# Kernel optimization log

Measured on AMD Instinct MI355X. Metric: run time of the kernel, lower is better.

## Reference

```python
import jax, jax.numpy as jnp
import numpy as np

RANK = 32
NC = 32                      # n_components = out_features / rank = 1024/32
TRI = RANK * (RANK + 1) // 2  # 528
EPS = 1e-5


def setup_inputs() -> dict:
    key = jax.random.key(0)
    k1, k2, k3, k4, k5 = jax.random.split(key, 5)
    B, T, D = 2, 2048, 1024
    param_arg = jax.random.normal(k1, (B, T, D), dtype=jnp.float32)
    input_arg = jax.random.normal(k2, (B, T, D), dtype=jnp.float32)
    # learned params (weight_norm linears collapse to plain weight matrices)
    W_uv = jax.random.normal(k3, (NC * TRI, D), dtype=jnp.float32) * 0.02
    W_alpha = jax.random.normal(k4, (NC, D), dtype=jnp.float32) * 0.02
    b_alpha = jax.random.normal(k5, (NC,), dtype=jnp.float32) * 0.02
    return {"param_arg": param_arg, "input_arg": input_arg,
            "W_uv": W_uv, "W_alpha": W_alpha, "b_alpha": b_alpha}


def reference(param_arg, input_arg, W_uv, W_alpha, b_alpha):
    B, T, D = input_arg.shape
    N = B * T * NC
    # projections (mixer_ac = identity)
    params = jnp.einsum('btd,pd->btp', param_arg, W_uv)            # [B,T,NC*TRI]
    alpha = jax.nn.sigmoid(jnp.einsum('btd,cd->btc', param_arg, W_alpha) + b_alpha)  # [B,T,NC]
    p = params.reshape(N, TRI)
    iu, ju = jnp.triu_indices(RANK)
    uv = jnp.zeros((N, RANK, RANK), dtype=p.dtype).at[:, iu, ju].set(p)
    uv = jnp.einsum('nij,nkj->nik', uv, uv)                        # U U^T, symmetric PSD
    # per-column L2 norm (dim=-2), then max over columns
    col = jnp.sqrt(jnp.sum(uv * uv, axis=-2, keepdims=True))       # [N,1,RANK]
    uv = uv / (jnp.max(col, axis=-1, keepdims=True) + EPS)
    x = input_arg.reshape(N, RANK)                                 # (-1, rank, 1)
    y = alpha.reshape(N, 1) * jnp.einsum('nij,nj->ni', uv, x)      # [N,RANK]
    return input_arg - y.reshape(B, T, D)
```

## Files before the change

kernel.cpp:

```cpp
#include <hip/hip_runtime.h>
#include <hip/hip_bf16.h>
#include <stdint.h>

typedef float f32x4 __attribute__((ext_vector_type(4)));
typedef float f32x16 __attribute__((ext_vector_type(16)));
typedef __bf16 bf16x8 __attribute__((ext_vector_type(8)));

#define EPS 1e-5f

static __device__ __forceinline__ unsigned short f2bf(float f) {
  unsigned int u = __float_as_uint(f);
  unsigned int r = (u + 0x7fffu + ((u >> 16) & 1u)) >> 16;
  return (unsigned short)r;
}

static __device__ __forceinline__ void gload_lds16(const unsigned short* g, unsigned short* s) {
  __builtin_amdgcn_global_load_lds((const __attribute__((address_space(1))) unsigned int*)g,
                                   (__attribute__((address_space(3))) unsigned int*)s,
                                   16, 0, 0);
}

__global__ void k_convert(const float* __restrict__ src, unsigned short* __restrict__ dst, int n4) {
  int idx = blockIdx.x * blockDim.x + threadIdx.x;
  int stride = gridDim.x * blockDim.x;
  for (int i = idx; i < n4; i += stride) {
    f32x4 v = ((const f32x4*)src)[i];
    ushort4 o;
    o.x = f2bf(v.x); o.y = f2bf(v.y); o.z = f2bf(v.z); o.w = f2bf(v.w);
    ((ushort4*)dst)[i] = o;
  }
}

__global__ __launch_bounds__(256) void k_alpha(const float* __restrict__ A,
                                               const float* __restrict__ Wa,
                                               const float* __restrict__ ba,
                                               float* __restrict__ alpha,
                                               unsigned short* __restrict__ Ab) {
  __shared__ __align__(16) float arow[1024];
  const int bt = blockIdx.x, tid = threadIdx.x;
  f32x4 v = ((const f32x4*)(A + (size_t)bt * 1024))[tid];
  ((f32x4*)arow)[tid] = v;
  ushort4 o;
  o.x = f2bf(v.x); o.y = f2bf(v.y); o.z = f2bf(v.z); o.w = f2bf(v.w);
  ((ushort4*)(Ab + (size_t)bt * 1024))[tid] = o;
  __syncthreads();
  const int c = tid >> 3, h = tid & 7;
  const float* wr = Wa + (size_t)c * 1024 + h * 128;
  const float* ar = arow + h * 128;
  float s = 0.f;
#pragma unroll 8
  for (int j = 0; j < 128; j += 4) {
    f32x4 wv = *(const f32x4*)(wr + j);
    s += wv.x * ar[j] + wv.y * ar[j + 1] + wv.z * ar[j + 2] + wv.w * ar[j + 3];
  }
  s += __shfl_down(s, 4);
  s += __shfl_down(s, 2);
  s += __shfl_down(s, 1);
  if (h == 0) {
    float z = s + ba[c];
    alpha[(size_t)bt * 32 + c] = 1.f / (1.f + __expf(-z));
  }
}

__global__ __launch_bounds__(256) void k_gemm(const unsigned short* __restrict__ A,
                                              const unsigned short* __restrict__ W,
                                              unsigned short* __restrict__ C) {
  __shared__ __align__(16) unsigned short As[4096];
  __shared__ __align__(16) unsigned short Bs[4096];
  const int bid = blockIdx.x;
  const int tm = bid / 132, tn = bid - tm * 132;
  const int m0 = tm << 7, n0 = tn << 7;
  const int tid = threadIdx.x;
  const int lane = tid & 63;
  const int w = tid >> 6;
  const int wm = w >> 1, wn = w & 1;
  const int fr = lane & 15, fq = lane >> 4;

  f32x4 acc[4][4];
#pragma unroll
  for (int i = 0; i < 4; ++i)
#pragma unroll
    for (int j = 0; j < 4; ++j) acc[i][j] = (f32x4){0.f, 0.f, 0.f, 0.f};

  const int srow = (w << 5) + (lane >> 2);
  const int scol = (lane & 3) << 3;
  const unsigned short* gA = A + (size_t)(m0 + srow) * 1024 + scol;
  const unsigned short* gB = W + (size_t)(n0 + srow) * 1024 + scol;

  for (int k0 = 0; k0 < 1024; k0 += 32) {
#pragma unroll
    for (int i = 0; i < 2; ++i) {
      gload_lds16(gA + (size_t)(i * 16) * 1024 + k0, &As[(w << 10) + (i << 9)]);
      gload_lds16(gB + (size_t)(i * 16) * 1024 + k0, &Bs[(w << 10) + (i << 9)]);
    }
    __syncthreads();
    bf16x8 af[4], bfr[4];
#pragma unroll
    for (int mi = 0; mi < 4; ++mi)
      af[mi] = *(const bf16x8*)&As[((wm << 6) + (mi << 4) + fr) * 32 + (fq << 3)];
#pragma unroll
    for (int ni = 0; ni < 4; ++ni)
      bfr[ni] = *(const bf16x8*)&Bs[((wn << 6) + (ni << 4) + fr) * 32 + (fq << 3)];
#pragma unroll
    for (int mi = 0; mi < 4; ++mi)
#pragma unroll
      for (int ni = 0; ni < 4; ++ni)
        acc[mi][ni] = __builtin_amdgcn_mfma_f32_16x16x32_bf16(af[mi], bfr[ni], acc[mi][ni], 0, 0, 0);
    __syncthreads();
  }

#pragma unroll
  for (int mi = 0; mi < 4; ++mi)
#pragma unroll
    for (int ni = 0; ni < 4; ++ni)
#pragma unroll
      for (int r = 0; r < 4; ++r) {
        int row = m0 + (wm << 6) + (mi << 4) + (fq << 2) + r;
        int col = n0 + (wn << 6) + (ni << 4) + fr;
        C[(size_t)row * 16896 + col] = f2bf(acc[mi][ni][r]);
      }
}

__global__ __launch_bounds__(256) void k_epi(const unsigned short* __restrict__ P,
                                             const float* __restrict__ X,
                                             const float* __restrict__ alpha,
                                             float* __restrict__ out) {
  __shared__ __align__(16) unsigned short U[4][1280];
  __shared__ __align__(16) float Xl[4][32];
  __shared__ unsigned short tab[528];
  const int tid = threadIdx.x;
  for (int e = tid; e < 528; e += 256) {
    float fi = (65.0f - sqrtf((float)(4225 - 8 * e))) * 0.5f;
    int i = (int)fi;
    int oi = (i * (65 - i)) >> 1;
    if (e < oi) { --i; oi = (i * (65 - i)) >> 1; }
    else { int oi1 = ((i + 1) * (64 - i)) >> 1; if (e >= oi1) { oi = oi1; ++i; } }
    tab[e] = (unsigned short)(i * 40 + i + (e - oi));
  }
  const int w = tid >> 6, lane = tid & 63;
  const int n = (blockIdx.x << 2) + w;
  const int bt = n >> 5, c = n & 31;
  unsigned short* Uw = U[w];
#pragma unroll
  for (int t = 0; t < 5; ++t) ((ushort4*)Uw)[lane + (t << 6)] = make_ushort4(0, 0, 0, 0);
  if (lane < 32) Xl[w][lane] = X[(size_t)bt * 1024 + (c << 5) + lane];
  __syncthreads();

  const unsigned short* p = P + (size_t)bt * 16896 + c * 528;
#pragma unroll
  for (int e = 0; e < 9; ++e) {
    int idx = lane + (e << 6);
    if (idx < 528) Uw[tab[idx]] = p[idx];
  }

  const int col = lane & 31, hi = lane >> 5;
  bf16x8 fa0 = *(const bf16x8*)&Uw[col * 40 + (hi << 3)];
  bf16x8 fa1 = *(const bf16x8*)&Uw[col * 40 + 16 + (hi << 3)];
  f32x16 S = {0.f, 0.f, 0.f, 0.f, 0.f, 0.f, 0.f, 0.f, 0.f, 0.f, 0.f, 0.f, 0.f, 0.f, 0.f, 0.f};
  S = __builtin_amdgcn_mfma_f32_32x32x16_bf16(fa0, fa0, S, 0, 0, 0);
  S = __builtin_amdgcn_mfma_f32_32x32x16_bf16(fa1, fa1, S, 0, 0, 0);

  float css = 0.f;
#pragma unroll
  for (int r = 0; r < 16; ++r) css += S[r] * S[r];
  css += __shfl_xor(css, 32);
  float m = css;
#pragma unroll
  for (int off = 1; off < 32; off <<= 1) m = fmaxf(m, __shfl_xor(m, off));
  m = sqrtf(m);
  const float scale = alpha[n] / (m + EPS);

  const float* xw = Xl[w];
  f32x4 x0 = *(const f32x4*)&xw[(hi << 2)];
  f32x4 x1 = *(const f32x4*)&xw[8 + (hi << 2)];
  f32x4 x2 = *(const f32x4*)&xw[16 + (hi << 2)];
  f32x4 x3 = *(const f32x4*)&xw[24 + (hi << 2)];
  float y = 0.f;
#pragma unroll
  for (int r = 0; r < 4; ++r) y += x0[r] * S[r];
#pragma unroll
  for (int r = 0; r < 4; ++r) y += x1[r] * S[4 + r];
#pragma unroll
  for (int r = 0; r < 4; ++r) y += x2[r] * S[8 + r];
#pragma unroll
  for (int r = 0; r < 4; ++r) y += x3[r] * S[12 + r];
  y += __shfl_xor(y, 32);

  if (hi == 0) {
    out[(size_t)bt * 1024 + (c << 5) + col] = xw[col] - scale * y;
  }
}

extern "C" void kernel_launch(void* const* d_in, const int* in_sizes, int n_in,
                              void* d_out, int out_size, void* d_ws, size_t ws_size,
                              hipStream_t stream) {
  const float* param = (const float*)d_in[0];
  const float* input = (const float*)d_in[1];
  const float* W_uv  = (const float*)d_in[2];
  const float* W_al  = (const float*)d_in[3];
  const float* b_al  = (const float*)d_in[4];
  float* out = (float*)d_out;

  char* ws = (char*)d_ws;
  unsigned short* Ab    = (unsigned short*)(ws);
  unsigned short* Wb    = (unsigned short*)(ws + 8388608);
  float*          alpha = (float*)(ws + 42991616);
  unsigned short* Pp    = (unsigned short*)(ws + 43515904);

  k_convert<<<4096, 256, 0, stream>>>(W_uv, Wb, (16896 * 1024) / 4);
  k_alpha<<<4096, 256, 0, stream>>>(param, W_al, b_al, alpha, Ab);
  k_gemm<<<32 * 132, 256, 0, stream>>>(Ab, Wb, Pp);
  k_epi<<<131072 / 4, 256, 0, stream>>>(Pp, input, alpha, out);
}
```

Measured before the change: 310.6 us.

## Replace bf16 GEMM with 256x256-tile double-buffered, swizzled, phase-pipelined kernel

```diff
diff --git a/kernel.cpp b/kernel.cpp
--- a/kernel.cpp
+++ b/kernel.cpp
@@ -62,62 +62,128 @@
   }
 }
 
-__global__ __launch_bounds__(256) void k_gemm(const unsigned short* __restrict__ A,
-                                              const unsigned short* __restrict__ W,
-                                              unsigned short* __restrict__ C) {
-  __shared__ __align__(16) unsigned short As[4096];
-  __shared__ __align__(16) unsigned short Bs[4096];
+
+#define SWZ(b) ((b) ^ ((((b) >> 9) & 3) << 5))
+
+#define STAGE(S, h) do {                                                        \
+  const int _buf = (S) & 1;                                                     \
+  const int _reg = _buf * 65536 + (((h) >= 2) ? ((h) - 2) * 16384               \
+                                              : 32768 + (h) * 16384);           \
+  const unsigned short* _mat = ((h) >= 2) ? A : W;                              \
+  const int _r0 = (((h) >= 2) ? m0 : n0) + ((h) & 1) * 128;                     \
+  const int _kb = (S) * 128;                                                    \
+  _Pragma("unroll")                                                             \
+  for (int _l = 0; _l < 2; ++_l) {                                              \
+    int _db = _l * 8192 + tid * 16;                                             \
+    int _sb = SWZ(_db);                                                         \
+    gload_lds16((const unsigned short*)((const char*)_mat +                     \
+                    (size_t)(_r0 + (_sb >> 7)) * 2048 + _kb + (_sb & 127)),     \
+                (unsigned short*)(smem + _reg + _l * 8192 + wid * 1024));       \
+  } } while (0)
+
+#define READ_A(buf, qm) do {                                                    \
+  _Pragma("unroll") for (int _mi = 0; _mi < 4; ++_mi)                           \
+  _Pragma("unroll") for (int _ks = 0; _ks < 2; ++_ks) {                         \
+    int _b = ((qm) * 64 + _mi * 16 + fr) * 128 + _ks * 64 + fq * 16;            \
+    _b = SWZ(_b);                                                               \
+    af[_mi][_ks] = *(const bf16x8*)(smem + (buf) * 65536 + wm * 16384 + _b);    \
+  } } while (0)
+
+#define READ_B(buf, qn) do {                                                    \
+  _Pragma("unroll") for (int _ni = 0; _ni < 2; ++_ni)                           \
+  _Pragma("unroll") for (int _ks = 0; _ks < 2; ++_ks) {                         \
+    int _b = ((wn & 1) * 64 + (qn) * 32 + _ni * 16 + fr) * 128 + _ks * 64 + fq * 16; \
+    _b = SWZ(_b);                                                               \
+    bfr[qn][_ni][_ks] = *(const bf16x8*)(smem + (buf) * 65536 + 32768 +         \
+                                         (wn >> 1) * 16384 + _b);               \
+  } } while (0)
+
+#define MMA(qm, qn) do {                                                        \
+  __builtin_amdgcn_s_setprio(1);                                                \
+  _Pragma("unroll") for (int _mi = 0; _mi < 4; ++_mi)                           \
+  _Pragma("unroll") for (int _ni = 0; _ni < 2; ++_ni)                           \
+  _Pragma("unroll") for (int _ks = 0; _ks < 2; ++_ks)                           \
+    acc[(qm) * 4 + _mi][(qn) * 2 + _ni] = __builtin_amdgcn_mfma_f32_16x16x32_bf16( \
+        af[_mi][_ks], bfr[qn][_ni][_ks], acc[(qm) * 4 + _mi][(qn) * 2 + _ni], 0, 0, 0); \
+  __builtin_amdgcn_s_setprio(0);                                                \
+  } while (0)
+
+#define PH_SYNC do {                                                            \
+  __builtin_amdgcn_s_barrier();                                                 \
+  asm volatile("s_waitcnt lgkmcnt(0)" ::: "memory");                            \
+  __builtin_amdgcn_sched_barrier(0);                                            \
+  } while (0)
+
+#define ENDBAR __builtin_amdgcn_s_barrier()
+#define VMW4 asm volatile("s_waitcnt vmcnt(4)" ::: "memory")
+#define LGKM8 asm volatile("s_waitcnt lgkmcnt(8)" ::: "memory")
+
+__global__ __launch_bounds__(512, 2) void k_gemm8(const unsigned short* __restrict__ A,
+                                                  const unsigned short* __restrict__ W,
+                                                  unsigned short* __restrict__ C) {
+  extern __shared__ char smem[];
   const int bid = blockIdx.x;
-  const int tm = bid / 132, tn = bid - tm * 132;
-  const int m0 = tm << 7, n0 = tn << 7;
+  const int tm = bid / 66, tn = bid - tm * 66;
+  const int m0 = tm << 8, n0 = tn << 8;
   const int tid = threadIdx.x;
   const int lane = tid & 63;
-  const int w = tid >> 6;
-  const int wm = w >> 1, wn = w & 1;
+  const int wid = tid >> 6;
+  const int wm = wid >> 2, wn = wid & 3;
   const int fr = lane & 15, fq = lane >> 4;
 
-  f32x4 acc[4][4];
-#pragma unroll
-  for (int i = 0; i < 4; ++i)
+  f32x4 acc[8][4];
+#pragma unroll
+  for (int i = 0; i < 8; ++i)
 #pragma unroll
     for (int j = 0; j < 4; ++j) acc[i][j] = (f32x4){0.f, 0.f, 0.f, 0.f};
 
-  const int srow = (w << 5) + (lane >> 2);
-  const int scol = (lane & 3) << 3;
-  const unsigned short* gA = A + (size_t)(m0 + srow) * 1024 + scol;
-  const unsigned short* gB = W + (size_t)(n0 + srow) * 1024 + scol;
-
-  for (int k0 = 0; k0 < 1024; k0 += 32) {
-#pragma unroll
-    for (int i = 0; i < 2; ++i) {
-      gload_lds16(gA + (size_t)(i * 16) * 1024 + k0, &As[(w << 10) + (i << 9)]);
-      gload_lds16(gB + (size_t)(i * 16) * 1024 + k0, &Bs[(w << 10) + (i << 9)]);
-    }
-    __syncthreads();
-    bf16x8 af[4], bfr[4];
-#pragma unroll
-    for (int mi = 0; mi < 4; ++mi)
-      af[mi] = *(const bf16x8*)&As[((wm << 6) + (mi << 4) + fr) * 32 + (fq << 3)];
-#pragma unroll
-    for (int ni = 0; ni < 4; ++ni)
-      bfr[ni] = *(const bf16x8*)&Bs[((wn << 6) + (ni << 4) + fr) * 32 + (fq << 3)];
-#pragma unroll
-    for (int mi = 0; mi < 4; ++mi)
-#pragma unroll
-      for (int ni = 0; ni < 4; ++ni)
-        acc[mi][ni] = __builtin_amdgcn_mfma_f32_16x16x32_bf16(af[mi], bfr[ni], acc[mi][ni], 0, 0, 0);
-    __syncthreads();
-  }
-
-#pragma unroll
-  for (int mi = 0; mi < 4; ++mi)
-#pragma unroll
-    for (int ni = 0; ni < 4; ++ni)
+  bf16x8 af[4][2];
+  bf16x8 bfr[2][2][2];
+
+  STAGE(0, 0); STAGE(0, 1); STAGE(0, 2); STAGE(0, 3);
+  STAGE(1, 0); STAGE(1, 1);
+  VMW4;
+  __builtin_amdgcn_s_barrier();
+
+  for (int i = 0; i < 8; ++i) {
+    const int S1 = 2 * i + 1, S2 = 2 * i + 2, S3 = 2 * i + 3;
+    READ_A(0, 0); READ_B(0, 0);
+    STAGE(S1, 2);
+    LGKM8;
+    PH_SYNC; MMA(0, 0); ENDBAR;
+    READ_B(0, 1);
+    STAGE(S1, 3);
+    PH_SYNC; MMA(0, 1); ENDBAR;
+    READ_A(0, 1);
+    if (i < 7) STAGE(S2, 0);
+    PH_SYNC; MMA(1, 0); ENDBAR;
+    if (i < 7) STAGE(S2, 1);
+    VMW4;
+    PH_SYNC; MMA(1, 1); ENDBAR;
+    READ_A(1, 0); READ_B(1, 0);
+    if (i < 7) STAGE(S2, 2);
+    LGKM8;
+    PH_SYNC; MMA(0, 0); ENDBAR;
+    READ_B(1, 1);
+    if (i < 7) STAGE(S2, 3);
+    PH_SYNC; MMA(0, 1); ENDBAR;
+    READ_A(1, 1);
+    if (i < 7) STAGE(S3, 0);
+    PH_SYNC; MMA(1, 0); ENDBAR;
+    if (i < 7) STAGE(S3, 1);
+    VMW4;
+    PH_SYNC; MMA(1, 1); ENDBAR;
+  }
+
+#pragma unroll
+  for (int am = 0; am < 8; ++am)
+#pragma unroll
+    for (int an = 0; an < 4; ++an)
 #pragma unroll
       for (int r = 0; r < 4; ++r) {
-        int row = m0 + (wm << 6) + (mi << 4) + (fq << 2) + r;
-        int col = n0 + (wn << 6) + (ni << 4) + fr;
-        C[(size_t)row * 16896 + col] = f2bf(acc[mi][ni][r]);
+        int row = m0 + (wm << 7) + (am << 4) + (fq << 2) + r;
+        int col = n0 + (wn << 6) + (an << 4) + fr;
+        C[(size_t)row * 16896 + col] = f2bf(acc[am][an][r]);
       }
 }
 
@@ -207,8 +273,11 @@
   float*          alpha = (float*)(ws + 42991616);
   unsigned short* Pp    = (unsigned short*)(ws + 43515904);
 
+  (void)hipFuncSetAttribute((const void*)k_gemm8,
+                            hipFuncAttributeMaxDynamicSharedMemorySize, 131072);
+
   k_convert<<<4096, 256, 0, stream>>>(W_uv, Wb, (16896 * 1024) / 4);
   k_alpha<<<4096, 256, 0, stream>>>(param, W_al, b_al, alpha, Ab);
-  k_gemm<<<32 * 132, 256, 0, stream>>>(Ab, Wb, Pp);
+  k_gemm8<<<16 * 66, 512, 131072, stream>>>(Ab, Wb, Pp);
   k_epi<<<131072 / 4, 256, 0, stream>>>(Pp, input, alpha, out);
 }
```

After: 544.9 us. +75.4%, slower.
